# Kernel tuning notes

Measured on AMD Instinct MI355X. Metric: run time of the kernel, lower is better.

Reference implementation:

```python
import jax, jax.numpy as jnp
import numpy as np

MARGIN = 0.3
EPS = 1e-6  # torch pairwise_distance eps inside triplet_margin_loss


def setup_inputs() -> dict:
    key = jax.random.key(0)
    k_e, k_l = jax.random.split(key)
    B, D, C = 8192, 128, 512
    emb = jax.random.normal(k_e, (B, D), dtype=jnp.float32)
    emb = emb / jnp.linalg.norm(emb, axis=-1, keepdims=True)  # docstring: L2-normalized
    labels = jax.random.randint(k_l, (B,), 0, C, dtype=jnp.int32)
    return {"embeddings": emb, "labels": labels}


def _pairwise_distances(emb):
    dot = emb @ emb.T                      # (B,B)
    sq = jnp.diagonal(dot)                 # (B,)
    d2 = sq[None, :] - 2.0 * dot + sq[:, None]
    return jnp.sqrt(jnp.clip(d2, 0.0))


def reference(embeddings, labels):
    B = embeddings.shape[0]
    # Mining uses distances only to produce indices -> no grad path in torch either.
    d = jax.lax.stop_gradient(_pairwise_distances(embeddings))

    same = labels[:, None] == labels[None, :]          # (B,B)
    eye = jnp.eye(B, dtype=bool)
    pos_mask = same & ~eye
    neg_mask = ~same
    valid = pos_mask.any(1) & neg_mask.any(1)           # anchors actually usable

    key = jax.random.key(42)
    kp, kn = jax.random.split(key)
    neg_inf = jnp.float32(-jnp.inf)

    # random positive per anchor via Gumbel-max over the positive mask
    gp = jax.random.gumbel(kp, (B, B), dtype=jnp.float32)
    pos_idx = jnp.argmax(jnp.where(pos_mask, gp, neg_inf), axis=1)   # (B,)
    ap = jnp.take_along_axis(d, pos_idx[:, None], axis=1)            # (B,1)

    # semi-hard negatives: ap < d(a,n) < ap + margin
    semi = neg_mask & (d > ap) & (d < ap + MARGIN)
    has_semi = semi.any(1)
    gn = jax.random.gumbel(kn, (B, B), dtype=jnp.float32)
    rand_semi = jnp.argmax(jnp.where(semi, gn, neg_inf), axis=1)
    hard_neg = jnp.argmin(jnp.where(neg_mask, d, jnp.inf), axis=1)   # fallback: hardest
    neg_idx = jnp.where(has_semi, rand_semi, hard_neg)

    a = embeddings
    p = embeddings[pos_idx]
    n = embeddings[neg_idx]
    dap = jnp.linalg.norm(a - p + EPS, axis=-1)
    dan = jnp.linalg.norm(a - n + EPS, axis=-1)
    per = jax.nn.relu(dap - dan + MARGIN)
    cnt = jnp.maximum(jnp.sum(valid.astype(jnp.float32)), 1.0)
    return jnp.sum(jnp.where(valid, per, 0.0)) / cnt
```

## Files before the change

kernel.cpp:

```cpp
#include <hip/hip_runtime.h>
#include <stdint.h>

#define B 8192
#define D 128
#define MARGIN 0.3f
#define EPS 1e-6f
#define HALFN (1u << 25)
#define NCHUNK 32
#define JCH (B / NCHUNK)
#define NPART 2048

using bf16x8 = __attribute__((ext_vector_type(8))) short;
using f32x16 = __attribute__((ext_vector_type(16))) float;

__host__ __device__ __forceinline__ void tf2x32(uint32_t k0, uint32_t k1,
                                                uint32_t x0, uint32_t x1,
                                                uint32_t& o0, uint32_t& o1) {
  uint32_t ks2 = k0 ^ k1 ^ 0x1BD11BDAu;
  uint32_t v0 = x0 + k0, v1 = x1 + k1;
#define RND(r) { v0 += v1; v1 = (v1 << (r)) | (v1 >> (32 - (r))); v1 ^= v0; }
  RND(13) RND(15) RND(26) RND(6)
  v0 += k1;  v1 += ks2 + 1u;
  RND(17) RND(29) RND(16) RND(24)
  v0 += ks2; v1 += k0 + 2u;
  RND(13) RND(15) RND(26) RND(6)
  v0 += k0;  v1 += k1 + 3u;
  RND(17) RND(29) RND(16) RND(24)
  v0 += k1;  v1 += ks2 + 4u;
  RND(13) RND(15) RND(26) RND(6)
  v0 += ks2; v1 += k0 + 5u;
#undef RND
  o0 = v0; o1 = v1;
}

__device__ __forceinline__ void tf_rounds(uint32_t k0, uint32_t k1,
                                          uint32_t v0, uint32_t v1,
                                          uint32_t& o0, uint32_t& o1) {
  uint32_t ks2 = k0 ^ k1 ^ 0x1BD11BDAu;
#define RNDL(r) { v0 += v1; v1 = __builtin_rotateleft32(v1, r); v1 ^= v0; }
  RNDL(13) RNDL(15) RNDL(26) RNDL(6)
  v0 += k1;  v1 += ks2 + 1u;
  RNDL(17) RNDL(29) RNDL(16) RNDL(24)
  v0 += ks2; v1 += k0 + 2u;
  RNDL(13) RNDL(15) RNDL(26) RNDL(6)
  v0 += k0;  v1 += k1 + 3u;
  RNDL(17) RNDL(29) RNDL(16) RNDL(24)
  v0 += k1;  v1 += ks2 + 4u;
  RNDL(13) RNDL(15) RNDL(26) RNDL(6)
  v0 += ks2; v1 += k0 + 5u;
#undef RNDL
  o0 = v0; o1 = v1;
}

__device__ __forceinline__ uint32_t gbits(uint32_t k0, uint32_t k1, uint32_t f) {
  bool lo = f < HALFN;
  uint32_t x0 = lo ? f : f - HALFN;
  uint32_t x1 = lo ? f + HALFN : f;
  uint32_t o0, o1;
  tf2x32(k0, k1, x0, x1, o0, o1);
  return (lo ? o0 : o1) >> 9;
}

__device__ __forceinline__ uint16_t f2bf(float f) {
  uint32_t u = __float_as_uint(f);
  return (uint16_t)((u + 0x7FFFu + ((u >> 16) & 1u)) >> 16);
}
__device__ __forceinline__ float bf2f(uint16_t b) {
  return __uint_as_float((uint32_t)b << 16);
}
__device__ __forceinline__ bf16x8 as_bf(uint4 u) {
  union { uint4 a; bf16x8 b; } x; x.a = u; return x.b;
}

__global__ __launch_bounds__(256) void prep_kernel(const float* __restrict__ emb,
                                                   uint32_t* __restrict__ chunk,
                                                   float* __restrict__ sq,
                                                   uint32_t* __restrict__ semikey,
                                                   uint32_t* __restrict__ hardkey) {
  int tid = blockIdx.x * 256 + threadIdx.x;
  int row = tid >> 4, oct = tid & 15;
  const float* src = emb + row * D + oct * 8;
  uint32_t hi[4], lo[4];
  float s = 0.0f;
  #pragma unroll
  for (int e = 0; e < 4; e++) {
    float f0 = src[2 * e], f1 = src[2 * e + 1];
    s = fmaf(f0, f0, s); s = fmaf(f1, f1, s);
    uint16_t h0 = f2bf(f0), h1 = f2bf(f1);
    uint16_t l0 = f2bf(__fsub_rn(f0, bf2f(h0)));
    uint16_t l1 = f2bf(__fsub_rn(f1, bf2f(h1)));
    hi[e] = (uint32_t)h0 | ((uint32_t)h1 << 16);
    lo[e] = (uint32_t)l0 | ((uint32_t)l1 << 16);
  }
  s += __shfl_xor(s, 1); s += __shfl_xor(s, 2);
  s += __shfl_xor(s, 4); s += __shfl_xor(s, 8);
  if (oct == 0) { sq[row] = s; semikey[row] = 0u; hardkey[row] = 0xFFFFFFFFu; }
  int g = row >> 5, kk = oct >> 1, lane = ((oct & 1) << 5) | (row & 31);
  uint32_t base = ((g * 8 + kk) * 2) * 64 + lane;
  *(uint4*)&chunk[(size_t)base * 4]        = make_uint4(hi[0], hi[1], hi[2], hi[3]);
  *(uint4*)&chunk[(size_t)(base + 64) * 4] = make_uint4(lo[0], lo[1], lo[2], lo[3]);
}

__global__ __launch_bounds__(256) void pos_kernel(
    const float* __restrict__ emb, const int* __restrict__ labels,
    const float* __restrict__ sq, uint32_t kp0, uint32_t kp1,
    int* __restrict__ posx, float* __restrict__ ap2lo, float* __restrict__ ap2hi,
    int* __restrict__ validf) {
  __shared__ int s_cnt[4];
  __shared__ int s_list[4][80];
  int wid = threadIdx.x >> 6, lane = threadIdx.x & 63;
  int i = blockIdx.x * 4 + wid;
  int lab = labels[i];
  if (lane == 0) s_cnt[wid] = 0;
  __syncthreads();
  for (int it = 0; it < B / 256; it++) {
    int j0 = it * 256 + lane * 4;
    int4 lv = *(const int4*)&labels[j0];
    #pragma unroll
    for (int e = 0; e < 4; e++) {
      if ((&lv.x)[e] == lab) {
        int pp = atomicAdd(&s_cnt[wid], 1);
        if (pp < 80) s_list[wid][pp] = j0 + e;
      }
    }
  }
  __syncthreads();
  int cnt = s_cnt[wid];

  uint32_t fbase = (uint32_t)i << 13;
  uint32_t bb = 0; int bi = -1;
  for (int t = lane; t < cnt; t += 64) {
    int j = s_list[wid][t];
    if (j != i) {
      uint32_t bits = gbits(kp0, kp1, fbase | (uint32_t)j);
      if (bi < 0 || bits > bb || (bits == bb && j < bi)) { bb = bits; bi = j; }
    }
  }
  #pragma unroll
  for (int off = 32; off > 0; off >>= 1) {
    uint32_t ob = __shfl_xor(bb, off);
    int oi = __shfl_xor(bi, off);
    if (oi >= 0 && (bi < 0 || ob > bb || (ob == bb && oi < bi))) { bb = ob; bi = oi; }
  }
  int pidx = (cnt >= 2) ? bi : 0;

  float a0 = emb[i * D + lane],    a1 = emb[i * D + 64 + lane];
  float p0 = emb[pidx * D + lane], p1 = emb[pidx * D + 64 + lane];
  float dot = fmaf(a1, p1, a0 * p0);
  #pragma unroll
  for (int off = 32; off > 0; off >>= 1) dot += __shfl_xor(dot, off);

  if (lane == 0) {
    float d2 = __fadd_rn(__fsub_rn(sq[pidx], __fmul_rn(2.0f, dot)), sq[i]);
    float apv = __fsqrt_rn(fmaxf(d2, 0.0f));
    float apm = __fadd_rn(apv, MARGIN);
    ap2lo[i] = __fmul_rn(apv, apv);
    ap2hi[i] = __fmul_rn(apm, apm);
    posx[i] = pidx;
    validf[i] = (cnt >= 2 && cnt < B) ? 1 : 0;
  }
}

__global__ __launch_bounds__(256, 3) void main_kernel(
    const uint32_t* __restrict__ chunk, const int* __restrict__ labels,
    const float* __restrict__ sq, const float* __restrict__ ap2lo,
    const float* __restrict__ ap2hi, uint32_t kn0, uint32_t kn1,
    uint32_t* __restrict__ semikey, uint32_t* __restrict__ hardkey) {
  __shared__ uint32_t ldsB[8192];
  __shared__ int s_labj[64];
  __shared__ float s_sqj4[64];

  const int tid = threadIdx.x;
  const int w = tid >> 6, lane = tid & 63;
  const int p = lane & 31, khalf = lane >> 5;
  const int A0 = blockIdx.x * 128;
  const int jc = blockIdx.y;
  const int ia_lo = A0 + 32 * w + p;
  const int ia_up = ia_lo + 4096;

  bf16x8 Af[2][8];
  {
    int g_lo = (A0 >> 5) + w;
    #pragma unroll
    for (int m = 0; m < 2; m++) {
      int g = g_lo + (m ? 128 : 0);
      #pragma unroll
      for (int kk = 0; kk < 8; kk++)
        Af[m][kk] = as_bf(*(const uint4*)&chunk[(size_t)(((g * 8 + kk) * 2) * 64 + lane) * 4]);
    }
  }

  const int lab_lo = labels[ia_lo], lab_up = labels[ia_up];
  const float sq_lo = sq[ia_lo], sq_up = sq[ia_up];
  const float Xlo_lo = __fadd_rn(__fsub_rn(ap2lo[ia_lo], sq_lo), 4.0f);
  const float Xhi_lo = __fadd_rn(__fsub_rn(ap2hi[ia_lo], sq_lo), 4.0f);
  const float Xlo_up = __fadd_rn(__fsub_rn(ap2lo[ia_up], sq_up), 4.0f);
  const float Xhi_up = __fadd_rn(__fsub_rn(ap2hi[ia_up], sq_up), 4.0f);
  const uint32_t c0 = ((uint32_t)ia_lo << 13) + kn0;
  const uint32_t c1 = ((uint32_t)ia_lo << 13) + HALFN + kn1;
  uint32_t sk_lo = 0u, sk_up = 0u;
  uint32_t hk_lo = 0xFFFFFFFFu, hk_up = 0xFFFFFFFFu;

  for (int jt = 0; jt < JCH; jt += 64) {
    const int jb = jc * JCH + jt;
    __syncthreads();
    {
      const uint32_t* src = chunk + (size_t)(jb >> 5) * 4096;
      #pragma unroll
      for (int q = 0; q < 8; q++) {
        int idx = tid + 256 * q;
        *(uint4*)&ldsB[idx * 4] = *(const uint4*)&src[idx * 4];
      }
      if (tid < 64) { s_labj[tid] = labels[jb + tid]; s_sqj4[tid] = sq[jb + tid] + 4.0f; }
    }
    __syncthreads();

    #pragma unroll
    for (int n0 = 0; n0 < 2; n0++) {
      f32x16 acc[2];
      acc[0] = (f32x16)(0.0f);
      acc[1] = (f32x16)(0.0f);

      #pragma unroll
      for (int kk = 0; kk < 8; kk++) {
        bf16x8 jh = *(const bf16x8*)&ldsB[(size_t)((n0 * 16 + kk * 2 + 0) * 64 + lane) * 4];
        bf16x8 jl = *(const bf16x8*)&ldsB[(size_t)((n0 * 16 + kk * 2 + 1) * 64 + lane) * 4];
        acc[0] = __builtin_amdgcn_mfma_f32_32x32x16_bf16(jh, Af[0][kk], acc[0], 0, 0, 0);
        acc[0] = __builtin_amdgcn_mfma_f32_32x32x16_bf16(jl, Af[0][kk], acc[0], 0, 0, 0);
        acc[1] = __builtin_amdgcn_mfma_f32_32x32x16_bf16(jh, Af[1][kk], acc[1], 0, 0, 0);
        acc[1] = __builtin_amdgcn_mfma_f32_32x32x16_bf16(jl, Af[1][kk], acc[1], 0, 0, 0);
      }

      #pragma unroll
      for (int g = 0; g < 4; g++) {
        uint32_t blo[4], bup[4];
        #pragma unroll
        for (int t = 0; t < 4; t++) {
          int row = t + (g << 3) + (khalf << 2);
          uint32_t jv = (uint32_t)(jb + n0 * 32 + row);
          uint32_t o0, o1;
          tf_rounds(kn0, kn1, c0 + jv, c1 + jv, o0, o1);
          blo[t] = o0 >> 13; bup[t] = o1 >> 13;
        }
        #pragma unroll
        for (int t = 0; t < 4; t++) {
          int r = (g << 2) + t;
          int row = t + (g << 3) + (khalf << 2);
          int jl_ = n0 * 32 + row;
          int j = jb + jl_;
          float sj4 = s_sqj4[jl_];
          int lj = s_labj[jl_];
          float Xl = fmaf(-2.0f, acc[0][r], sj4);
          float Xu = fmaf(-2.0f, acc[1][r], sj4);
          bool nl = (lj != lab_lo), nu = (lj != lab_up);
          uint32_t rj = (uint32_t)(8191 - j);
          uint32_t keyl = (blo[t] << 13) | rj;
          uint32_t keyu = (bup[t] << 13) | rj;
          bool il = nl && (Xl > Xlo_lo) && (Xl < Xhi_lo);
          bool iu = nu && (Xu > Xlo_up) && (Xu < Xhi_up);
          uint32_t csl = il ? keyl : 0u;
          uint32_t csu = iu ? keyu : 0u;
          sk_lo = max(sk_lo, csl);
          sk_up = max(sk_up, csu);
          uint32_t hl = nl ? ((__float_as_uint(Xl) & 0xFFFFE000u) | (uint32_t)j) : 0xFFFFFFFFu;
          uint32_t hu = nu ? ((__float_as_uint(Xu) & 0xFFFFE000u) | (uint32_t)j) : 0xFFFFFFFFu;
          hk_lo = min(hk_lo, hl);
          hk_up = min(hk_up, hu);
        }
      }
    }
  }

  {
    uint32_t o;
    o = __shfl_xor(sk_lo, 32); sk_lo = max(sk_lo, o);
    o = __shfl_xor(sk_up, 32); sk_up = max(sk_up, o);
    o = __shfl_xor(hk_lo, 32); hk_lo = min(hk_lo, o);
    o = __shfl_xor(hk_up, 32); hk_up = min(hk_up, o);
  }
  if (lane < 32) {
    atomicMax(&semikey[ia_lo], sk_lo);
    atomicMin(&hardkey[ia_lo], hk_lo);
  } else {
    atomicMax(&semikey[ia_up], sk_up);
    atomicMin(&hardkey[ia_up], hk_up);
  }
}

__global__ __launch_bounds__(256) void finalize_kernel(
    const float* __restrict__ emb, const int* __restrict__ posx,
    const int* __restrict__ validf,
    const uint32_t* __restrict__ semikey, const uint32_t* __restrict__ hardkey,
    float* __restrict__ pers, float* __restrict__ cnts) {
  __shared__ float s_per[4];
  __shared__ float s_cnt[4];
  int wid = threadIdx.x >> 6, lane = threadIdx.x & 63;
  int i = blockIdx.x * 4 + wid;

  uint32_t sk = semikey[i];
  uint32_t hk = hardkey[i];
  int neg = sk ? (8191 - (int)(sk & 8191u)) : (int)(hk & 8191u);
  if (!sk && hk == 0xFFFFFFFFu) neg = 0;
  int pos = posx[i];

  float sap = 0.0f, san = 0.0f;
  #pragma unroll
  for (int k = lane; k < D; k += 64) {
    float a = emb[i * D + k];
    float dp = __fadd_rn(__fsub_rn(a, emb[pos * D + k]), EPS);
    float dn = __fadd_rn(__fsub_rn(a, emb[neg * D + k]), EPS);
    sap = fmaf(dp, dp, sap);
    san = fmaf(dn, dn, san);
  }
  #pragma unroll
  for (int off = 32; off > 0; off >>= 1) {
    sap += __shfl_down(sap, off);
    san += __shfl_down(san, off);
  }
  if (lane == 0) {
    int v = validf[i];
    float per = __fadd_rn(__fsub_rn(__fsqrt_rn(sap), __fsqrt_rn(san)), MARGIN);
    per = fmaxf(per, 0.0f);
    s_per[wid] = v ? per : 0.0f;
    s_cnt[wid] = v ? 1.0f : 0.0f;
  }
  __syncthreads();
  if (threadIdx.x == 0) {
    pers[blockIdx.x] = s_per[0] + s_per[1] + s_per[2] + s_per[3];
    cnts[blockIdx.x] = s_cnt[0] + s_cnt[1] + s_cnt[2] + s_cnt[3];
  }
}

__global__ __launch_bounds__(256) void reduce_kernel(
    const float* __restrict__ pers, const float* __restrict__ cnts,
    float* __restrict__ out) {
  __shared__ float rp[256], rcn[256];
  int tid = threadIdx.x;
  float sp = 0.0f, sc = 0.0f;
  #pragma unroll
  for (int q = 0; q < NPART / 256; q++) {
    sp += pers[tid + 256 * q];
    sc += cnts[tid + 256 * q];
  }
  rp[tid] = sp; rcn[tid] = sc;
  __syncthreads();
  for (int s = 128; s > 0; s >>= 1) {
    if (tid < s) { rp[tid] += rp[tid + s]; rcn[tid] += rcn[tid + s]; }
    __syncthreads();
  }
  if (tid == 0) out[0] = rp[0] / fmaxf(rcn[0], 1.0f);
}

extern "C" void kernel_launch(void* const* d_in, const int* in_sizes, int n_in,
                              void* d_out, int out_size, void* d_ws, size_t ws_size,
                              hipStream_t stream) {
  const float* emb = (const float*)d_in[0];
  const int* labels = (const int*)d_in[1];
  char* ws = (char*)d_ws;
  float* sq        = (float*)(ws + 0);
  float* ap2lo     = (float*)(ws + 32768);
  float* ap2hi     = (float*)(ws + 65536);
  int* posx        = (int*)(ws + 98304);
  int* validf      = (int*)(ws + 131072);
  float* pers      = (float*)(ws + 163840);
  float* cnts      = (float*)(ws + 180224);
  uint32_t* semikey= (uint32_t*)(ws + 196608);
  uint32_t* hardkey= (uint32_t*)(ws + 229376);
  uint32_t* chnk   = (uint32_t*)(ws + 262144);
  float* out       = (float*)d_out;

  uint32_t A0, B0, A1, B1;
  tf2x32(0u, 42u, 0u, 2u, A0, B0);
  tf2x32(0u, 42u, 1u, 3u, A1, B1);
  uint32_t kp0 = A0, kp1 = A1, kn0 = B0, kn1 = B1;

  prep_kernel<<<512, 256, 0, stream>>>(emb, chnk, sq, semikey, hardkey);
  pos_kernel<<<B / 4, 256, 0, stream>>>(emb, labels, sq, kp0, kp1, posx, ap2lo, ap2hi, validf);
  main_kernel<<<dim3(32, NCHUNK), 256, 0, stream>>>(chnk, labels, sq, ap2lo, ap2hi,
                                                    kn0, kn1, semikey, hardkey);
  finalize_kernel<<<NPART, 256, 0, stream>>>(emb, posx, validf, semikey, hardkey,
                                             pers, cnts);
  reduce_kernel<<<1, 256, 0, stream>>>(pers, cnts, out);
}
```

Measured before the change: 168.6 us.

## Fuse prep into pos kernel, fold final reduce into finalize, double j-chunks

Merges the prep and positive-mining kernels into one launch, computing the anchor and positive squared norms locally instead of reading sq. Folds the final reduction into finalize_kernel using an atomic ticket, so the last block does the sum. Doubles NCHUNK so main_kernel launches twice as many blocks, each with a shorter j range. It also packs the label and norm into one float2 LDS entry and simplifies key construction. Together these cut launch count and raise main-kernel parallelism, at the cost of more atomics on semikey/hardkey.

```diff
diff --git a/kernel.cpp b/kernel.cpp
--- a/kernel.cpp
+++ b/kernel.cpp
@@ -6,7 +6,7 @@
 #define MARGIN 0.3f
 #define EPS 1e-6f
 #define HALFN (1u << 25)
-#define NCHUNK 32
+#define NCHUNK 64
 #define JCH (B / NCHUNK)
 #define NPART 2048
 
@@ -72,46 +72,48 @@
   union { uint4 a; bf16x8 b; } x; x.a = u; return x.b;
 }
 
-__global__ __launch_bounds__(256) void prep_kernel(const float* __restrict__ emb,
-                                                   uint32_t* __restrict__ chunk,
-                                                   float* __restrict__ sq,
-                                                   uint32_t* __restrict__ semikey,
-                                                   uint32_t* __restrict__ hardkey) {
-  int tid = blockIdx.x * 256 + threadIdx.x;
-  int row = tid >> 4, oct = tid & 15;
-  const float* src = emb + row * D + oct * 8;
-  uint32_t hi[4], lo[4];
-  float s = 0.0f;
-  #pragma unroll
-  for (int e = 0; e < 4; e++) {
-    float f0 = src[2 * e], f1 = src[2 * e + 1];
-    s = fmaf(f0, f0, s); s = fmaf(f1, f1, s);
-    uint16_t h0 = f2bf(f0), h1 = f2bf(f1);
-    uint16_t l0 = f2bf(__fsub_rn(f0, bf2f(h0)));
-    uint16_t l1 = f2bf(__fsub_rn(f1, bf2f(h1)));
-    hi[e] = (uint32_t)h0 | ((uint32_t)h1 << 16);
-    lo[e] = (uint32_t)l0 | ((uint32_t)l1 << 16);
-  }
-  s += __shfl_xor(s, 1); s += __shfl_xor(s, 2);
-  s += __shfl_xor(s, 4); s += __shfl_xor(s, 8);
-  if (oct == 0) { sq[row] = s; semikey[row] = 0u; hardkey[row] = 0xFFFFFFFFu; }
-  int g = row >> 5, kk = oct >> 1, lane = ((oct & 1) << 5) | (row & 31);
-  uint32_t base = ((g * 8 + kk) * 2) * 64 + lane;
-  *(uint4*)&chunk[(size_t)base * 4]        = make_uint4(hi[0], hi[1], hi[2], hi[3]);
-  *(uint4*)&chunk[(size_t)(base + 64) * 4] = make_uint4(lo[0], lo[1], lo[2], lo[3]);
-}
-
-__global__ __launch_bounds__(256) void pos_kernel(
+__global__ __launch_bounds__(256) void pp_kernel(
     const float* __restrict__ emb, const int* __restrict__ labels,
-    const float* __restrict__ sq, uint32_t kp0, uint32_t kp1,
+    uint32_t kp0, uint32_t kp1,
+    uint32_t* __restrict__ chunk, float* __restrict__ sq,
     int* __restrict__ posx, float* __restrict__ ap2lo, float* __restrict__ ap2hi,
-    int* __restrict__ validf) {
+    int* __restrict__ validf,
+    uint32_t* __restrict__ semikey, uint32_t* __restrict__ hardkey,
+    uint32_t* __restrict__ ticket) {
   __shared__ int s_cnt[4];
   __shared__ int s_list[4][80];
   int wid = threadIdx.x >> 6, lane = threadIdx.x & 63;
   int i = blockIdx.x * 4 + wid;
+
+  if (blockIdx.x == 0 && threadIdx.x == 0) *ticket = 0u;
+  if (lane == 0) { semikey[i] = 0u; hardkey[i] = 0xFFFFFFFFu; s_cnt[wid] = 0; }
+
+  if (blockIdx.x < 512) {
+    int tid = blockIdx.x * 256 + threadIdx.x;
+    int row = tid >> 4, oct = tid & 15;
+    const float* src = emb + row * D + oct * 8;
+    uint32_t hi[4], lo[4];
+    float s = 0.0f;
+    #pragma unroll
+    for (int e = 0; e < 4; e++) {
+      float f0 = src[2 * e], f1 = src[2 * e + 1];
+      s = fmaf(f0, f0, s); s = fmaf(f1, f1, s);
+      uint16_t h0 = f2bf(f0), h1 = f2bf(f1);
+      uint16_t l0 = f2bf(__fsub_rn(f0, bf2f(h0)));
+      uint16_t l1 = f2bf(__fsub_rn(f1, bf2f(h1)));
+      hi[e] = (uint32_t)h0 | ((uint32_t)h1 << 16);
+      lo[e] = (uint32_t)l0 | ((uint32_t)l1 << 16);
+    }
+    s += __shfl_xor(s, 1); s += __shfl_xor(s, 2);
+    s += __shfl_xor(s, 4); s += __shfl_xor(s, 8);
+    if (oct == 0) sq[row] = s;
+    int g = row >> 5, kk = oct >> 1, ln = ((oct & 1) << 5) | (row & 31);
+    uint32_t base = ((g * 8 + kk) * 2) * 64 + ln;
+    *(uint4*)&chunk[(size_t)base * 4]        = make_uint4(hi[0], hi[1], hi[2], hi[3]);
+    *(uint4*)&chunk[(size_t)(base + 64) * 4] = make_uint4(lo[0], lo[1], lo[2], lo[3]);
+  }
+
   int lab = labels[i];
-  if (lane == 0) s_cnt[wid] = 0;
   __syncthreads();
   for (int it = 0; it < B / 256; it++) {
     int j0 = it * 256 + lane * 4;
@@ -147,11 +149,17 @@
   float a0 = emb[i * D + lane],    a1 = emb[i * D + 64 + lane];
   float p0 = emb[pidx * D + lane], p1 = emb[pidx * D + 64 + lane];
   float dot = fmaf(a1, p1, a0 * p0);
+  float sqi = fmaf(a1, a1, a0 * a0);
+  float sqp = fmaf(p1, p1, p0 * p0);
   #pragma unroll
-  for (int off = 32; off > 0; off >>= 1) dot += __shfl_xor(dot, off);
+  for (int off = 32; off > 0; off >>= 1) {
+    dot += __shfl_xor(dot, off);
+    sqi += __shfl_xor(sqi, off);
+    sqp += __shfl_xor(sqp, off);
+  }
 
   if (lane == 0) {
-    float d2 = __fadd_rn(__fsub_rn(sq[pidx], __fmul_rn(2.0f, dot)), sq[i]);
+    float d2 = __fadd_rn(__fsub_rn(sqp, __fmul_rn(2.0f, dot)), sqi);
     float apv = __fsqrt_rn(fmaxf(d2, 0.0f));
     float apm = __fadd_rn(apv, MARGIN);
     ap2lo[i] = __fmul_rn(apv, apv);
@@ -167,8 +175,7 @@
     const float* __restrict__ ap2hi, uint32_t kn0, uint32_t kn1,
     uint32_t* __restrict__ semikey, uint32_t* __restrict__ hardkey) {
   __shared__ uint32_t ldsB[8192];
-  __shared__ int s_labj[64];
-  __shared__ float s_sqj4[64];
+  __shared__ float2 s_ji[64];
 
   const int tid = threadIdx.x;
   const int w = tid >> 6, lane = tid & 63;
@@ -211,7 +218,8 @@
         int idx = tid + 256 * q;
         *(uint4*)&ldsB[idx * 4] = *(const uint4*)&src[idx * 4];
       }
-      if (tid < 64) { s_labj[tid] = labels[jb + tid]; s_sqj4[tid] = sq[jb + tid] + 4.0f; }
+      if (tid < 64)
+        s_ji[tid] = make_float2(sq[jb + tid] + 4.0f, __int_as_float(labels[jb + tid]));
     }
     __syncthreads();
 
@@ -233,14 +241,12 @@
 
       #pragma unroll
       for (int g = 0; g < 4; g++) {
-        uint32_t blo[4], bup[4];
+        uint32_t olo[4], oup[4];
         #pragma unroll
         for (int t = 0; t < 4; t++) {
           int row = t + (g << 3) + (khalf << 2);
           uint32_t jv = (uint32_t)(jb + n0 * 32 + row);
-          uint32_t o0, o1;
-          tf_rounds(kn0, kn1, c0 + jv, c1 + jv, o0, o1);
-          blo[t] = o0 >> 13; bup[t] = o1 >> 13;
+          tf_rounds(kn0, kn1, c0 + jv, c1 + jv, olo[t], oup[t]);
         }
         #pragma unroll
         for (int t = 0; t < 4; t++) {
@@ -248,14 +254,14 @@
           int row = t + (g << 3) + (khalf << 2);
           int jl_ = n0 * 32 + row;
           int j = jb + jl_;
-          float sj4 = s_sqj4[jl_];
-          int lj = s_labj[jl_];
-          float Xl = fmaf(-2.0f, acc[0][r], sj4);
-          float Xu = fmaf(-2.0f, acc[1][r], sj4);
+          float2 ji = s_ji[jl_];
+          int lj = __float_as_int(ji.y);
+          float Xl = fmaf(-2.0f, acc[0][r], ji.x);
+          float Xu = fmaf(-2.0f, acc[1][r], ji.x);
           bool nl = (lj != lab_lo), nu = (lj != lab_up);
           uint32_t rj = (uint32_t)(8191 - j);
-          uint32_t keyl = (blo[t] << 13) | rj;
-          uint32_t keyu = (bup[t] << 13) | rj;
+          uint32_t keyl = (olo[t] & 0xFFFFE000u) | rj;
+          uint32_t keyu = (oup[t] & 0xFFFFE000u) | rj;
           bool il = nl && (Xl > Xlo_lo) && (Xl < Xhi_lo);
           bool iu = nu && (Xu > Xlo_up) && (Xu < Xhi_up);
           uint32_t csl = il ? keyl : 0u;
@@ -291,9 +297,12 @@
     const float* __restrict__ emb, const int* __restrict__ posx,
     const int* __restrict__ validf,
     const uint32_t* __restrict__ semikey, const uint32_t* __restrict__ hardkey,
-    float* __restrict__ pers, float* __restrict__ cnts) {
+    float* __restrict__ pers, float* __restrict__ cnts,
+    uint32_t* __restrict__ ticket, float* __restrict__ out) {
   __shared__ float s_per[4];
   __shared__ float s_cnt[4];
+  __shared__ float s_rp[4], s_rc[4];
+  __shared__ int s_last;
   int wid = threadIdx.x >> 6, lane = threadIdx.x & 63;
   int i = blockIdx.x * 4 + wid;
 
@@ -328,27 +337,30 @@
   if (threadIdx.x == 0) {
     pers[blockIdx.x] = s_per[0] + s_per[1] + s_per[2] + s_per[3];
     cnts[blockIdx.x] = s_cnt[0] + s_cnt[1] + s_cnt[2] + s_cnt[3];
-  }
-}
-
-__global__ __launch_bounds__(256) void reduce_kernel(
-    const float* __restrict__ pers, const float* __restrict__ cnts,
-    float* __restrict__ out) {
-  __shared__ float rp[256], rcn[256];
-  int tid = threadIdx.x;
-  float sp = 0.0f, sc = 0.0f;
-  #pragma unroll
-  for (int q = 0; q < NPART / 256; q++) {
-    sp += pers[tid + 256 * q];
-    sc += cnts[tid + 256 * q];
-  }
-  rp[tid] = sp; rcn[tid] = sc;
+    __threadfence();
+    uint32_t t = atomicAdd(ticket, 1u);
+    s_last = (t == NPART - 1) ? 1 : 0;
+  }
   __syncthreads();
-  for (int s = 128; s > 0; s >>= 1) {
-    if (tid < s) { rp[tid] += rp[tid + s]; rcn[tid] += rcn[tid + s]; }
+  if (s_last) {
+    __threadfence();
+    volatile const float* vp = pers;
+    volatile const float* vc = cnts;
+    float sp = 0.0f, sc = 0.0f;
+    for (int q = threadIdx.x; q < NPART; q += 256) { sp += vp[q]; sc += vc[q]; }
+    #pragma unroll
+    for (int off = 32; off > 0; off >>= 1) {
+      sp += __shfl_down(sp, off);
+      sc += __shfl_down(sc, off);
+    }
+    if (lane == 0) { s_rp[wid] = sp; s_rc[wid] = sc; }
     __syncthreads();
-  }
-  if (tid == 0) out[0] = rp[0] / fmaxf(rcn[0], 1.0f);
+    if (threadIdx.x == 0) {
+      float tp = s_rp[0] + s_rp[1] + s_rp[2] + s_rp[3];
+      float tc = s_rc[0] + s_rc[1] + s_rc[2] + s_rc[3];
+      out[0] = tp / fmaxf(tc, 1.0f);
+    }
+  }
 }
 
 extern "C" void kernel_launch(void* const* d_in, const int* in_sizes, int n_in,
@@ -363,9 +375,10 @@
   int* posx        = (int*)(ws + 98304);
   int* validf      = (int*)(ws + 131072);
   float* pers      = (float*)(ws + 163840);
-  float* cnts      = (float*)(ws + 180224);
-  uint32_t* semikey= (uint32_t*)(ws + 196608);
-  uint32_t* hardkey= (uint32_t*)(ws + 229376);
+  float* cnts      = (float*)(ws + 172032);
+  uint32_t* semikey= (uint32_t*)(ws + 180224);
+  uint32_t* hardkey= (uint32_t*)(ws + 212992);
+  uint32_t* ticket = (uint32_t*)(ws + 245760);
   uint32_t* chnk   = (uint32_t*)(ws + 262144);
   float* out       = (float*)d_out;
 
@@ -374,11 +387,11 @@
   tf2x32(0u, 42u, 1u, 3u, A1, B1);
   uint32_t kp0 = A0, kp1 = A1, kn0 = B0, kn1 = B1;
 
-  prep_kernel<<<512, 256, 0, stream>>>(emb, chnk, sq, semikey, hardkey);
-  pos_kernel<<<B / 4, 256, 0, stream>>>(emb, labels, sq, kp0, kp1, posx, ap2lo, ap2hi, validf);
+  pp_kernel<<<NPART, 256, 0, stream>>>(emb, labels, kp0, kp1, chnk, sq,
+                                       posx, ap2lo, ap2hi, validf,
+                                       semikey, hardkey, ticket);
   main_kernel<<<dim3(32, NCHUNK), 256, 0, stream>>>(chnk, labels, sq, ap2lo, ap2hi,
                                                     kn0, kn1, semikey, hardkey);
   finalize_kernel<<<NPART, 256, 0, stream>>>(emb, posx, validf, semikey, hardkey,
-                                             pers, cnts);
-  reduce_kernel<<<1, 256, 0, stream>>>(pers, cnts, out);
-}
+                                             pers, cnts, ticket, out);
+}
```

New measurement: 204.4 us. +21.2%, slower.

## Double main-kernel chunk count, share label scan across waves, pack per-column LDS data

Applied to the files above, without the earlier changes.

Raises NCHUNK from 32 to 64 so main_kernel launches twice as many blocks, each covering half as many columns. This adds parallelism across the GPU, at the cost of more partial-key reductions and redundant A-fragment loads. In pos_kernel, all 256 threads now scan the label array once and compare against all four wave labels, instead of each wave scanning the full array on its own. It also packs each column's squared norm and label into one float2 LDS entry, replaces a shift pair with a mask when building the random keys, and repacks workspace offsets.

```diff
diff --git a/kernel.cpp b/kernel.cpp
--- a/kernel.cpp
+++ b/kernel.cpp
@@ -6,7 +6,7 @@
 #define MARGIN 0.3f
 #define EPS 1e-6f
 #define HALFN (1u << 25)
-#define NCHUNK 32
+#define NCHUNK 64
 #define JCH (B / NCHUNK)
 #define NPART 2048
 
@@ -107,21 +107,24 @@
     int* __restrict__ posx, float* __restrict__ ap2lo, float* __restrict__ ap2hi,
     int* __restrict__ validf) {
   __shared__ int s_cnt[4];
+  __shared__ int s_lab4[4];
   __shared__ int s_list[4][80];
   int wid = threadIdx.x >> 6, lane = threadIdx.x & 63;
   int i = blockIdx.x * 4 + wid;
-  int lab = labels[i];
-  if (lane == 0) s_cnt[wid] = 0;
+  if (lane == 0) { s_cnt[wid] = 0; s_lab4[wid] = labels[i]; }
   __syncthreads();
-  for (int it = 0; it < B / 256; it++) {
-    int j0 = it * 256 + lane * 4;
+  int l0 = s_lab4[0], l1 = s_lab4[1], l2 = s_lab4[2], l3 = s_lab4[3];
+  #pragma unroll
+  for (int it = 0; it < B / 1024; it++) {
+    int j0 = it * 1024 + threadIdx.x * 4;
     int4 lv = *(const int4*)&labels[j0];
     #pragma unroll
     for (int e = 0; e < 4; e++) {
-      if ((&lv.x)[e] == lab) {
-        int pp = atomicAdd(&s_cnt[wid], 1);
-        if (pp < 80) s_list[wid][pp] = j0 + e;
-      }
+      int l = (&lv.x)[e];
+      if (l == l0) { int pp = atomicAdd(&s_cnt[0], 1); if (pp < 80) s_list[0][pp] = j0 + e; }
+      if (l == l1) { int pp = atomicAdd(&s_cnt[1], 1); if (pp < 80) s_list[1][pp] = j0 + e; }
+      if (l == l2) { int pp = atomicAdd(&s_cnt[2], 1); if (pp < 80) s_list[2][pp] = j0 + e; }
+      if (l == l3) { int pp = atomicAdd(&s_cnt[3], 1); if (pp < 80) s_list[3][pp] = j0 + e; }
     }
   }
   __syncthreads();
@@ -167,8 +170,7 @@
     const float* __restrict__ ap2hi, uint32_t kn0, uint32_t kn1,
     uint32_t* __restrict__ semikey, uint32_t* __restrict__ hardkey) {
   __shared__ uint32_t ldsB[8192];
-  __shared__ int s_labj[64];
-  __shared__ float s_sqj4[64];
+  __shared__ float2 s_ji[64];
 
   const int tid = threadIdx.x;
   const int w = tid >> 6, lane = tid & 63;
@@ -211,7 +213,8 @@
         int idx = tid + 256 * q;
         *(uint4*)&ldsB[idx * 4] = *(const uint4*)&src[idx * 4];
       }
-      if (tid < 64) { s_labj[tid] = labels[jb + tid]; s_sqj4[tid] = sq[jb + tid] + 4.0f; }
+      if (tid < 64)
+        s_ji[tid] = make_float2(sq[jb + tid] + 4.0f, __int_as_float(labels[jb + tid]));
     }
     __syncthreads();
 
@@ -233,14 +236,12 @@
 
       #pragma unroll
       for (int g = 0; g < 4; g++) {
-        uint32_t blo[4], bup[4];
+        uint32_t olo[4], oup[4];
         #pragma unroll
         for (int t = 0; t < 4; t++) {
           int row = t + (g << 3) + (khalf << 2);
           uint32_t jv = (uint32_t)(jb + n0 * 32 + row);
-          uint32_t o0, o1;
-          tf_rounds(kn0, kn1, c0 + jv, c1 + jv, o0, o1);
-          blo[t] = o0 >> 13; bup[t] = o1 >> 13;
+          tf_rounds(kn0, kn1, c0 + jv, c1 + jv, olo[t], oup[t]);
         }
         #pragma unroll
         for (int t = 0; t < 4; t++) {
@@ -248,14 +249,14 @@
           int row = t + (g << 3) + (khalf << 2);
           int jl_ = n0 * 32 + row;
           int j = jb + jl_;
-          float sj4 = s_sqj4[jl_];
-          int lj = s_labj[jl_];
-          float Xl = fmaf(-2.0f, acc[0][r], sj4);
-          float Xu = fmaf(-2.0f, acc[1][r], sj4);
+          float2 ji = s_ji[jl_];
+          int lj = __float_as_int(ji.y);
+          float Xl = fmaf(-2.0f, acc[0][r], ji.x);
+          float Xu = fmaf(-2.0f, acc[1][r], ji.x);
           bool nl = (lj != lab_lo), nu = (lj != lab_up);
           uint32_t rj = (uint32_t)(8191 - j);
-          uint32_t keyl = (blo[t] << 13) | rj;
-          uint32_t keyu = (bup[t] << 13) | rj;
+          uint32_t keyl = (olo[t] & 0xFFFFE000u) | rj;
+          uint32_t keyu = (oup[t] & 0xFFFFE000u) | rj;
           bool il = nl && (Xl > Xlo_lo) && (Xl < Xhi_lo);
           bool iu = nu && (Xu > Xlo_up) && (Xu < Xhi_up);
           uint32_t csl = il ? keyl : 0u;
@@ -363,9 +364,9 @@
   int* posx        = (int*)(ws + 98304);
   int* validf      = (int*)(ws + 131072);
   float* pers      = (float*)(ws + 163840);
-  float* cnts      = (float*)(ws + 180224);
-  uint32_t* semikey= (uint32_t*)(ws + 196608);
-  uint32_t* hardkey= (uint32_t*)(ws + 229376);
+  float* cnts      = (float*)(ws + 172032);
+  uint32_t* semikey= (uint32_t*)(ws + 180224);
+  uint32_t* hardkey= (uint32_t*)(ws + 212992);
   uint32_t* chnk   = (uint32_t*)(ws + 262144);
   float* out       = (float*)d_out;
 
```

Result: no change. 167.7 us (-0.6%).
